# Optimization experiments

Measured on AMD Instinct MI355X. Metric: run time of the kernel, lower is better.

## Reference

```python
import jax, jax.numpy as jnp
import numpy as np

H, W = 480, 640
NUM_CLASSES = 3
SKIP = 5            # skip_pixels: stride between voting pixels
GRID = 8            # stride of Hough accumulator bins
LABEL_THRESHOLD = 5
INLIER_THRESHOLD = 0.5
VOTING_THRESHOLD = 0.3


def setup_inputs():
    key = jax.random.key(0)
    k1, k2, k3, k4 = jax.random.split(key, 4)
    bottom_label = jax.random.randint(k1, (1, H, W), 0, NUM_CLASSES).astype(jnp.int32)
    bottom_vertex = jax.random.normal(k2, (1, NUM_CLASSES * 3, H, W), jnp.float32)
    bottom_meta_data = jax.random.normal(k3, (1, 10), jnp.float32)
    extents = jax.random.normal(k4, (NUM_CLASSES, 3), jnp.float32)
    return {"bottom_label": bottom_label, "bottom_vertex": bottom_vertex,
            "bottom_meta_data": bottom_meta_data, "extents": extents}


def _hough_voting(bottom_label, bottom_vertex, bottom_meta_data, extents):
    label = bottom_label[0]                                   # [H,W] int
    vert = bottom_vertex[0].reshape(NUM_CLASSES, 3, H, W)     # per-class (ux,uy,dist)

    # voter pixels on a SKIP-strided grid
    vy, vx = jnp.meshgrid(jnp.arange(0, H, SKIP), jnp.arange(0, W, SKIP), indexing="ij")
    vy = vy.reshape(-1)
    vx = vx.reshape(-1)                                       # [V]
    vl = label[vy, vx]                                        # voter class labels [V]
    d = vert[vl, :, vy, vx]                                   # [V,3] gather own-class prediction
    ux, uy, dist = d[:, 0], d[:, 1], d[:, 2]

    # Hough bin centers on a GRID-strided grid
    by, bx = jnp.meshgrid(jnp.arange(GRID // 2, H, GRID), jnp.arange(GRID // 2, W, GRID), indexing="ij")
    by = by.reshape(-1).astype(jnp.float32)
    bx = bx.reshape(-1).astype(jnp.float32)                   # [B]

    # per (voter, bin) agreement between predicted direction and vector to bin
    ddx = bx[None, :] - vx[:, None].astype(jnp.float32)       # [V,B]
    ddy = by[None, :] - vy[:, None].astype(jnp.float32)
    inv_n = jax.lax.rsqrt(ddx * ddx + ddy * ddy + 1e-6)
    cos = (ddx * ux[:, None] + ddy * uy[:, None]) * inv_n     # [V,B]
    w = jnp.where((cos > INLIER_THRESHOLD) & (vl[:, None] > 0), 1.0, 0.0)

    # scatter votes into per-class Hough space (class 0 = background, masked above)
    hough = jax.ops.segment_sum(w, vl, num_segments=NUM_CLASSES)                 # [C,B]
    dsum = jax.ops.segment_sum(w * dist[:, None], vl, num_segments=NUM_CLASSES)  # [C,B]
    counts = jax.ops.segment_sum(jnp.ones_like(vl, jnp.float32), vl, num_segments=NUM_CLASSES)

    # peak detection per class
    peak = jnp.argmax(hough, axis=1)                          # [C]
    votes = jnp.take_along_axis(hough, peak[:, None], axis=1)[:, 0]
    depth = jnp.take_along_axis(dsum, peak[:, None], axis=1)[:, 0] / jnp.maximum(votes, 1.0)
    cx = bx[peak]
    cy = by[peak]
    score = votes / jnp.maximum(counts, 1.0)
    valid = (counts > LABEL_THRESHOLD) & (score > VOTING_THRESHOLD)

    # project object extents through camera intrinsics at estimated depth -> box size
    fx = bottom_meta_data[0, 0]
    fy = bottom_meta_data[0, 4]
    diag = jnp.sqrt(jnp.sum(extents * extents, axis=1))       # [C]
    safe_z = jnp.maximum(jnp.abs(depth), 1e-3)
    bw = jnp.abs(diag * fx) / safe_z
    bh = jnp.abs(diag * fy) / safe_z

    cls = jnp.arange(NUM_CLASSES, dtype=jnp.float32)
    rois = jnp.stack([cls, cx - bw / 2, cy - bh / 2, cx + bw / 2, cy + bh / 2,
                      score * valid.astype(jnp.float32)], axis=1)  # [C,6]
    return rois, hough


def reference(bottom_label, bottom_vertex, bottom_meta_data, extents):
    return _hough_voting(bottom_label, bottom_vertex, bottom_meta_data, extents)
```

## Files before the change

kernel.cpp:

```cpp
#include <hip/hip_runtime.h>

#define HH 480
#define WW 640
#define NC 3
#define NVX 128
#define NVY 96
#define NV (NVX * NVY)
#define NBX 80
#define NBY 60
#define NB (NBX * NBY)
#define CHUNK 128
#define NCHUNK (NV / CHUNK)
#define BINBLOCKS ((NB + 255) / 256)
#define NPB 96

__global__ void precompute_pts(const int* __restrict__ label,
                               const float* __restrict__ vert,
                               float4* __restrict__ ptsA,
                               float4* __restrict__ ptsB,
                               float* __restrict__ hough,
                               float* __restrict__ dsum,
                               float* __restrict__ blockCounts) {
    __shared__ int hist[NC];
    const int tid = threadIdx.x;
    if (tid < NC) hist[tid] = 0;
    __syncthreads();
    const int i = blockIdx.x * 256 + tid;
    if (i < NV) {
        int iy = i >> 7;
        int ix = i & (NVX - 1);
        int pix = (5 * iy) * WW + 5 * ix;
        int vl = label[pix];
        const float* base = vert + (size_t)(vl * 3) * HH * WW + pix;
        float ux = base[0];
        float uy = base[(size_t)HH * WW];
        float dist = base[(size_t)2 * HH * WW];
        ptsA[i] = make_float4((float)(5 * ix), (float)(5 * iy), ux, uy);
        float c1 = (vl == 1) ? 1.0f : 0.0f;
        float c2 = (vl == 2) ? 1.0f : 0.0f;
        ptsB[i] = make_float4((vl == 1) ? dist : 0.0f,
                              (vl == 2) ? dist : 0.0f, c1, c2);
        atomicAdd(&hist[vl], 1);
    }
    if (i < NC * NB) hough[i] = 0.0f;
    if (i < 2 * NB) dsum[i] = 0.0f;
    __syncthreads();
    if (tid < NC) blockCounts[blockIdx.x * NC + tid] = (float)hist[tid];
}

__global__ void vote(const float4* __restrict__ ptsA,
                     const float4* __restrict__ ptsB,
                     float* __restrict__ hough,
                     float* __restrict__ dsum) {
    __shared__ float4 shA[CHUNK];
    __shared__ float4 shB[CHUNK];
    const int tid = threadIdx.x;
    const int p0 = blockIdx.y * CHUNK;
    if (tid < CHUNK) shA[tid] = ptsA[p0 + tid];
    else             shB[tid - CHUNK] = ptsB[p0 + tid - CHUNK];

    const int b = blockIdx.x * 256 + tid;
    const float bxf = (float)(4 + 8 * (b % NBX));
    const float byf = (float)(4 + 8 * (b / NBX));
    float h1 = 0.f, h2 = 0.f, d1 = 0.f, d2 = 0.f;
    __syncthreads();

#pragma unroll 4
    for (int j = 0; j < CHUNK; ++j) {
        float4 a = shA[j];
        float4 q = shB[j];
        float ddx = bxf - a.x;
        float ddy = byf - a.y;
        float nx  = __builtin_fmaf(ddx, ddx, __builtin_fmaf(ddy, ddy, 1e-6f));
        float inv = __builtin_amdgcn_rsqf(nx);
        float dot = __builtin_fmaf(ddx, a.z, ddy * a.w);
        float t   = dot * inv - 0.5f;
        if (fabsf(t) < 1e-4f) {
            float nxe  = __fadd_rn(__fadd_rn(__fmul_rn(ddx, ddx),
                                             __fmul_rn(ddy, ddy)), 1e-6f);
            float inve = __fdiv_rn(1.0f, __fsqrt_rn(nxe));
            float dote = __fadd_rn(__fmul_rn(ddx, a.z), __fmul_rn(ddy, a.w));
            t = __fmul_rn(dote, inve) - 0.5f;
        }
        float m = (t > 0.0f) ? 1.0f : 0.0f;
        d1 = __builtin_fmaf(m, q.x, d1);
        d2 = __builtin_fmaf(m, q.y, d2);
        h1 = __builtin_fmaf(m, q.z, h1);
        h2 = __builtin_fmaf(m, q.w, h2);
    }
    if (b < NB) {
        atomicAdd(&hough[NB + b], h1);
        atomicAdd(&hough[2 * NB + b], h2);
        atomicAdd(&dsum[b], d1);
        atomicAdd(&dsum[NB + b], d2);
    }
}

__global__ void finalize(const float* __restrict__ hough,
                         const float* __restrict__ dsum,
                         const float* __restrict__ blockCounts,
                         const float* __restrict__ meta,
                         const float* __restrict__ extents,
                         float* __restrict__ rois) {
    __shared__ unsigned long long skey[256];
    __shared__ float scnt[256];
    const int tid = threadIdx.x;
    const int c = blockIdx.x;

    float cnt = 0.0f;
    for (int i = tid; i < NPB; i += 256) cnt += blockCounts[i * NC + c];
    scnt[tid] = cnt;

    unsigned long long best = 0ull;
    for (int i = tid; i < NB; i += 256) {
        float v = hough[c * NB + i];
        unsigned long long key =
            ((unsigned long long)__float_as_uint(v) << 32) |
            (unsigned long long)(unsigned)(NB - 1 - i);
        if (key > best) best = key;
    }
    skey[tid] = best;
    __syncthreads();
    for (int s = 128; s > 0; s >>= 1) {
        if (tid < s) {
            if (skey[tid + s] > skey[tid]) skey[tid] = skey[tid + s];
            scnt[tid] += scnt[tid + s];
        }
        __syncthreads();
    }
    if (tid == 0) {
        float votes = __uint_as_float((unsigned)(skey[0] >> 32));
        int peak = NB - 1 - (int)(skey[0] & 0xffffffffull);
        float ds = (c == 0) ? 0.0f : dsum[(c - 1) * NB + peak];
        float depth = __fdiv_rn(ds, fmaxf(votes, 1.0f));
        float cx = (float)(4 + 8 * (peak % NBX));
        float cy = (float)(4 + 8 * (peak / NBX));
        float cntf = scnt[0];
        float score = __fdiv_rn(votes, fmaxf(cntf, 1.0f));
        int valid = (cntf > 5.0f) && (score > 0.3f);
        float fx = meta[0], fy = meta[4];
        float e0 = extents[c * 3 + 0];
        float e1 = extents[c * 3 + 1];
        float e2 = extents[c * 3 + 2];
        float diag = __fsqrt_rn(__fadd_rn(
            __fadd_rn(__fmul_rn(e0, e0), __fmul_rn(e1, e1)), __fmul_rn(e2, e2)));
        float sz = fmaxf(fabsf(depth), 0.001f);
        float bw = __fdiv_rn(fabsf(__fmul_rn(diag, fx)), sz);
        float bh = __fdiv_rn(fabsf(__fmul_rn(diag, fy)), sz);
        rois[c * 6 + 0] = (float)c;
        rois[c * 6 + 1] = cx - bw * 0.5f;
        rois[c * 6 + 2] = cy - bh * 0.5f;
        rois[c * 6 + 3] = cx + bw * 0.5f;
        rois[c * 6 + 4] = cy + bh * 0.5f;
        rois[c * 6 + 5] = valid ? score : 0.0f;
    }
}

extern "C" void kernel_launch(void* const* d_in, const int* in_sizes, int n_in,
                              void* d_out, int out_size, void* d_ws, size_t ws_size,
                              hipStream_t stream) {
    const int* label = (const int*)d_in[0];
    const float* vert = (const float*)d_in[1];
    const float* meta = (const float*)d_in[2];
    const float* extents = (const float*)d_in[3];
    float* out = (float*)d_out;

    char* ws = (char*)d_ws;
    float4* ptsA = (float4*)ws;
    float4* ptsB = (float4*)(ws + (size_t)NV * 16);
    float* dsum = (float*)(ws + (size_t)2 * NV * 16);
    float* blockCounts = (float*)(ws + (size_t)2 * NV * 16 + 2 * NB * 4);

    float* hough = out + NC * 6;

    precompute_pts<<<NPB, 256, 0, stream>>>(label, vert, ptsA, ptsB,
                                            hough, dsum, blockCounts);
    vote<<<dim3(BINBLOCKS, NCHUNK), 256, 0, stream>>>(ptsA, ptsB, hough, dsum);
    finalize<<<NC, 256, 0, stream>>>(hough, dsum, blockCounts, meta, extents, out);
}
```

Baseline: 103.0 us.

## Compact foreground voters per block and replace rsqrt with squared cosine test

The precompute kernel now uses wave ballots and prefix counts to pack only foreground voters (label > 0) into each 256-entry chunk, and writes a per-chunk count. The vote kernel loops only over that count, so background voters that contribute nothing are skipped. Vote chunks grow from 128 to 256 entries, which halves the number of chunk blocks. The inlier test cos > 0.5 becomes dot > 0 and dot² > 0.25·|d|², removing the rsqrt, with an exact fallback near the boundary. This adds a data-dependent loop bound and some divergence near the threshold.

New measurement: 101.3 us. Within noise of the previous version (-1.7%).

```diff
diff --git a/kernel.cpp b/kernel.cpp
--- a/kernel.cpp
+++ b/kernel.cpp
@@ -9,55 +9,70 @@
 #define NBX 80
 #define NBY 60
 #define NB (NBX * NBY)
-#define CHUNK 128
-#define NCHUNK (NV / CHUNK)
+#define NPB 48
 #define BINBLOCKS ((NB + 255) / 256)
-#define NPB 96
 
 __global__ void precompute_pts(const int* __restrict__ label,
                                const float* __restrict__ vert,
                                float4* __restrict__ ptsA,
                                float4* __restrict__ ptsB,
+                               int* __restrict__ cnt,
+                               float* __restrict__ blockCounts,
                                float* __restrict__ hough,
-                               float* __restrict__ dsum,
-                               float* __restrict__ blockCounts) {
-    __shared__ int hist[NC];
+                               float* __restrict__ dsum) {
+    __shared__ int swtot[4], sn2[4];
     const int tid = threadIdx.x;
-    if (tid < NC) hist[tid] = 0;
+    const int i = blockIdx.x * 256 + tid;
+    const int iy = i >> 7;
+    const int ix = i & (NVX - 1);
+    const int pix = (5 * iy) * WW + 5 * ix;
+    const int vl = label[pix];
+    const float* base = vert + (size_t)(vl * 3) * HH * WW + pix;
+    const float ux = base[0];
+    const float uy = base[(size_t)HH * WW];
+    const float dist = base[(size_t)2 * HH * WW];
+
+    const bool pos = (vl > 0);
+    const int lane = tid & 63, w = tid >> 6;
+    unsigned long long mp = __ballot(pos);
+    unsigned long long m2 = __ballot(vl == 2);
+    int rank = __popcll(mp & ((1ull << lane) - 1ull));
+    if (lane == 0) { swtot[w] = __popcll(mp); sn2[w] = __popcll(m2); }
     __syncthreads();
-    const int i = blockIdx.x * 256 + tid;
-    if (i < NV) {
-        int iy = i >> 7;
-        int ix = i & (NVX - 1);
-        int pix = (5 * iy) * WW + 5 * ix;
-        int vl = label[pix];
-        const float* base = vert + (size_t)(vl * 3) * HH * WW + pix;
-        float ux = base[0];
-        float uy = base[(size_t)HH * WW];
-        float dist = base[(size_t)2 * HH * WW];
-        ptsA[i] = make_float4((float)(5 * ix), (float)(5 * iy), ux, uy);
-        float c1 = (vl == 1) ? 1.0f : 0.0f;
+    int off = 0;
+    for (int k = 0; k < w; ++k) off += swtot[k];
+    if (pos) {
+        int p = blockIdx.x * 256 + off + rank;
+        ptsA[p] = make_float4((float)(5 * ix), (float)(5 * iy), ux, uy);
         float c2 = (vl == 2) ? 1.0f : 0.0f;
-        ptsB[i] = make_float4((vl == 1) ? dist : 0.0f,
-                              (vl == 2) ? dist : 0.0f, c1, c2);
-        atomicAdd(&hist[vl], 1);
+        ptsB[p] = make_float4((vl == 1) ? dist : 0.0f,
+                              (vl == 2) ? dist : 0.0f,
+                              (vl == 1) ? 1.0f : 0.0f, c2);
     }
-    if (i < NC * NB) hough[i] = 0.0f;
+    if (tid == 0) {
+        int tot = swtot[0] + swtot[1] + swtot[2] + swtot[3];
+        int n2 = sn2[0] + sn2[1] + sn2[2] + sn2[3];
+        cnt[blockIdx.x] = tot;
+        blockCounts[blockIdx.x * NC + 0] = (float)(256 - tot);
+        blockCounts[blockIdx.x * NC + 1] = (float)(tot - n2);
+        blockCounts[blockIdx.x * NC + 2] = (float)n2;
+    }
+    for (int k = i; k < NC * NB; k += NV) hough[k] = 0.0f;
     if (i < 2 * NB) dsum[i] = 0.0f;
-    __syncthreads();
-    if (tid < NC) blockCounts[blockIdx.x * NC + tid] = (float)hist[tid];
 }
 
 __global__ void vote(const float4* __restrict__ ptsA,
                      const float4* __restrict__ ptsB,
+                     const int* __restrict__ cnt,
                      float* __restrict__ hough,
                      float* __restrict__ dsum) {
-    __shared__ float4 shA[CHUNK];
-    __shared__ float4 shB[CHUNK];
+    __shared__ float4 shA[256];
+    __shared__ float4 shB[256];
     const int tid = threadIdx.x;
-    const int p0 = blockIdx.y * CHUNK;
-    if (tid < CHUNK) shA[tid] = ptsA[p0 + tid];
-    else             shB[tid - CHUNK] = ptsB[p0 + tid - CHUNK];
+    const int p0 = blockIdx.y * 256;
+    shA[tid] = ptsA[p0 + tid];
+    shB[tid] = ptsB[p0 + tid];
+    const int n = cnt[blockIdx.y];
 
     const int b = blockIdx.x * 256 + tid;
     const float bxf = (float)(4 + 8 * (b % NBX));
@@ -66,23 +81,23 @@
     __syncthreads();
 
 #pragma unroll 4
-    for (int j = 0; j < CHUNK; ++j) {
+    for (int j = 0; j < n; ++j) {
         float4 a = shA[j];
         float4 q = shB[j];
         float ddx = bxf - a.x;
         float ddy = byf - a.y;
         float nx  = __builtin_fmaf(ddx, ddx, __builtin_fmaf(ddy, ddy, 1e-6f));
-        float inv = __builtin_amdgcn_rsqf(nx);
         float dot = __builtin_fmaf(ddx, a.z, ddy * a.w);
-        float t   = dot * inv - 0.5f;
-        if (fabsf(t) < 1e-4f) {
+        float s   = __builtin_fmaf(dot, dot, -0.25f * nx);
+        bool v = (dot > 0.0f) & (s > 0.0f);
+        if (__builtin_expect((dot > 0.0f) && (fabsf(s) < nx * 2e-5f), 0)) {
             float nxe  = __fadd_rn(__fadd_rn(__fmul_rn(ddx, ddx),
                                              __fmul_rn(ddy, ddy)), 1e-6f);
             float inve = __fdiv_rn(1.0f, __fsqrt_rn(nxe));
             float dote = __fadd_rn(__fmul_rn(ddx, a.z), __fmul_rn(ddy, a.w));
-            t = __fmul_rn(dote, inve) - 0.5f;
+            v = __fmul_rn(dote, inve) > 0.5f;
         }
-        float m = (t > 0.0f) ? 1.0f : 0.0f;
+        float m = v ? 1.0f : 0.0f;
         d1 = __builtin_fmaf(m, q.x, d1);
         d2 = __builtin_fmaf(m, q.y, d2);
         h1 = __builtin_fmaf(m, q.z, h1);
@@ -107,9 +122,9 @@
     const int tid = threadIdx.x;
     const int c = blockIdx.x;
 
-    float cnt = 0.0f;
-    for (int i = tid; i < NPB; i += 256) cnt += blockCounts[i * NC + c];
-    scnt[tid] = cnt;
+    float cntv = 0.0f;
+    for (int i = tid; i < NPB; i += 256) cntv += blockCounts[i * NC + c];
+    scnt[tid] = cntv;
 
     unsigned long long best = 0ull;
     for (int i = tid; i < NB; i += 256) {
@@ -170,11 +185,12 @@
     float4* ptsB = (float4*)(ws + (size_t)NV * 16);
     float* dsum = (float*)(ws + (size_t)2 * NV * 16);
     float* blockCounts = (float*)(ws + (size_t)2 * NV * 16 + 2 * NB * 4);
+    int* cnt = (int*)(ws + (size_t)2 * NV * 16 + 2 * NB * 4 + NPB * NC * 4);
 
     float* hough = out + NC * 6;
 
     precompute_pts<<<NPB, 256, 0, stream>>>(label, vert, ptsA, ptsB,
-                                            hough, dsum, blockCounts);
-    vote<<<dim3(BINBLOCKS, NCHUNK), 256, 0, stream>>>(ptsA, ptsB, hough, dsum);
+                                            cnt, blockCounts, hough, dsum);
+    vote<<<dim3(BINBLOCKS, NPB), 256, 0, stream>>>(ptsA, ptsB, cnt, hough, dsum);
     finalize<<<NC, 256, 0, stream>>>(hough, dsum, blockCounts, meta, extents, out);
 }
```
